# Performance work log

Measured on AMD Instinct MI355X. Metric: run time of the kernel, lower is better.

## Reference

```python
import jax, jax.numpy as jnp
import numpy as np

N = 50000   # nodes
E = 800000  # edges per metapath
P = 3       # num_meta_paths
H = 4       # heads
D = 64      # out_size per head
IN = H * D  # in_size = 256 (required by residual g_emb.flatten(1) + h)
EPS = 1e-5
NEG_SLOPE = 0.2  # DGL GATConv leaky_relu default


def setup_inputs() -> dict:
    key = jax.random.key(0)
    ks = jax.random.split(key, 7)
    h = jax.random.normal(ks[0], (N, IN), jnp.float32)
    path_mask = jnp.ones((N, P), jnp.float32)
    src = jax.random.randint(ks[1], (P, E), 0, N, jnp.int32)
    dst = jax.random.randint(ks[2], (P, E), 0, N, jnp.int32)
    # per-metapath GATConv params (bias=False)
    fc_w = jax.random.normal(ks[3], (P, IN, H * D), jnp.float32) * 0.05
    attn_l = jax.random.normal(ks[4], (P, H, D), jnp.float32) * 0.05
    attn_r = jax.random.normal(ks[5], (P, H, D), jnp.float32) * 0.05
    bn_gamma = jnp.ones((IN,), jnp.float32)
    bn_beta = jnp.zeros((IN,), jnp.float32)
    return {"h": h, "path_mask": path_mask, "src": src, "dst": dst,
            "fc_w": fc_w, "attn_l": attn_l, "attn_r": attn_r,
            "bn_gamma": bn_gamma, "bn_beta": bn_beta}


def _gat(h, src, dst, w, al, ar):
    # DGL GATConv: linear proj, additive attention, edge-softmax over dst neighborhoods
    feat = (h @ w).reshape(N, H, D)                       # [N,H,D]
    el = jnp.sum(feat * al, axis=-1)                      # [N,H]
    er = jnp.sum(feat * ar, axis=-1)                      # [N,H]
    e = jax.nn.leaky_relu(el[src] + er[dst], NEG_SLOPE)   # [E,H]
    # numerically-stable segment softmax over incoming edges of each dst node
    m = jax.ops.segment_max(e, dst, num_segments=N)       # [N,H]
    ex = jnp.exp(e - m[dst])
    denom = jax.ops.segment_sum(ex, dst, num_segments=N)  # [N,H]
    alpha = ex / denom[dst]                               # [E,H]
    out = jax.ops.segment_sum(alpha[:, :, None] * feat[src], dst, num_segments=N)  # [N,H,D]
    return jax.nn.relu(out), alpha


def _bn(x, gamma, beta):
    # BatchNorm1d in training mode: batch statistics over node dim
    mu = jnp.mean(x, axis=0)
    var = jnp.var(x, axis=0)
    return gamma * (x - mu) * jax.lax.rsqrt(var + EPS) + beta


def reference(h, path_mask, src, dst, fc_w, attn_l, attn_r, bn_gamma, bn_beta):
    embs, attns = [], []
    for p in range(P):
        o, a = _gat(h, src[p], dst[p], fc_w[p], attn_l[p], attn_r[p])
        embs.append(_bn(o.reshape(N, H * D) + h, bn_gamma, bn_beta))
        attns.append(jnp.mean(a, axis=1))  # mean over heads -> per-edge coef [E]
    sem = jnp.stack(embs, axis=1)                              # [N,P,IN]
    w = path_mask / jnp.sum(path_mask, axis=1, keepdims=True)  # masked mean weights [N,P]
    pooled = jnp.einsum('np,npd->nd', w, sem)                  # [N,IN]
    gat_attns = jnp.stack(attns)                               # [P,E] (sparse values; indices = src/dst)
    return pooled, w, gat_attns
```

## Files before the change

### kernel.cpp

```cpp
#include <hip/hip_runtime.h>
#include <stdint.h>

#define N_NODES 50000
#define N_EDGES 800000
#define N_PATHS 3
#define N_HEADS 4
#define IN_F 256
#define BN_EPS 1e-5f
#define NEG_SLOPE 0.2f
#define CAP 48
#define NB_PER_PATH 49
#define NB_TOT (N_PATHS * NB_PER_PATH)
#define REC_CAP 18432
#define BIN_EPB 4096
#define TOT_EDGES (N_PATHS * N_EDGES)
#define BIN_BLOCKS ((TOT_EDGES + BIN_EPB - 1) / BIN_EPB)

typedef short bf16x8 __attribute__((ext_vector_type(8)));
typedef float f32x4 __attribute__((ext_vector_type(4)));

__device__ inline unsigned short f2bf(float f) {
  unsigned u = __float_as_uint(f);
  unsigned r = (u + 0x7FFFu + ((u >> 16) & 1u)) >> 16;
  return (unsigned short)r;
}
__device__ inline float bf2f(unsigned short s) {
  return __uint_as_float(((unsigned)s) << 16);
}
__device__ inline float bfl(unsigned u) { return __uint_as_float(u << 16); }
__device__ inline float bfh(unsigned u) { return __uint_as_float(u & 0xFFFF0000u); }

__global__ __launch_bounds__(256) void k_zero(unsigned* p, int nwords) {
  int i = blockIdx.x * 256 + threadIdx.x;
  if (i < nwords) p[i] = 0u;
}

__global__ __launch_bounds__(256) void k_convert_w(const float* __restrict__ fcw,
                                                   unsigned short* __restrict__ wbf) {
  __shared__ float sh[32][33];
  int bt = blockIdx.x;
  int p = bt >> 6;
  int tile = bt & 63;
  int tk = tile >> 3, tn = tile & 7;
  const float* base = fcw + (size_t)p * IN_F * IN_F;
  unsigned short* ob = wbf + (size_t)p * IN_F * IN_F;
  int c = threadIdx.x & 31, r0 = threadIdx.x >> 5;
  #pragma unroll
  for (int it = 0; it < 4; ++it) {
    int r = r0 + it * 8;
    sh[r][c] = base[(size_t)(tk * 32 + r) * IN_F + tn * 32 + c];
  }
  __syncthreads();
  #pragma unroll
  for (int it = 0; it < 4; ++it) {
    int r = r0 + it * 8;
    ob[(size_t)(tn * 32 + r) * IN_F + tk * 32 + c] = f2bf(sh[c][r]);
  }
}

__global__ __launch_bounds__(256) void k_bin(const int* __restrict__ src, const int* __restrict__ dst,
                                             unsigned* __restrict__ gcurP, unsigned* __restrict__ grec) {
  __shared__ unsigned hist[NB_TOT];
  __shared__ unsigned lbase[NB_TOT];
  __shared__ unsigned gbase[NB_TOT];
  __shared__ unsigned lcur[NB_TOT];
  __shared__ unsigned scanbuf[256];
  __shared__ unsigned char sbuck[BIN_EPB];
  __shared__ unsigned stage[BIN_EPB];
  int t = threadIdx.x;
  int base = blockIdx.x * BIN_EPB;
  for (int i = t; i < NB_TOT; i += 256) { hist[i] = 0u; lcur[i] = 0u; }
  __syncthreads();

  unsigned rec[16];
  int bk[16];
  #pragma unroll
  for (int k = 0; k < 16; ++k) {
    int gid = base + t + k * 256;
    bk[k] = -1;
    if (gid < TOT_EDGES) {
      int s = src[gid], d = dst[gid];
      int p = (gid >= 2 * N_EDGES) ? 2 : ((gid >= N_EDGES) ? 1 : 0);
      int b = p * NB_PER_PATH + (d >> 10);
      bk[k] = b;
      rec[k] = (unsigned)s | ((unsigned)(d & 1023) << 17);
      atomicAdd(&hist[b], 1u);
    }
  }
  __syncthreads();
  for (int i = t; i < NB_TOT; i += 256)
    gbase[i] = hist[i] ? atomicAdd(&gcurP[i * 16], hist[i]) : 0u;
  scanbuf[t] = (t < NB_TOT) ? hist[t] : 0u;
  __syncthreads();
  for (int off = 1; off < 256; off <<= 1) {
    unsigned v = (t >= off) ? scanbuf[t - off] : 0u;
    __syncthreads();
    scanbuf[t] += v;
    __syncthreads();
  }
  if (t < NB_TOT) lbase[t] = scanbuf[t] - hist[t];
  __syncthreads();
  #pragma unroll
  for (int k = 0; k < 16; ++k) {
    if (bk[k] >= 0) {
      int b = bk[k];
      unsigned pos = atomicAdd(&lcur[b], 1u) + lbase[b];
      stage[pos] = rec[k];
      sbuck[pos] = (unsigned char)b;
    }
  }
  __syncthreads();
  int nblk = TOT_EDGES - base;
  if (nblk > BIN_EPB) nblk = BIN_EPB;
  for (int i = t; i < nblk; i += 256) {
    int b = sbuck[i];
    unsigned off = (unsigned)i - lbase[b];
    unsigned gpos = gbase[b] + off;
    if (gpos < REC_CAP) grec[(size_t)b * REC_CAP + gpos] = stage[i];
  }
}

__global__ __launch_bounds__(1024) void k_fine(const unsigned* __restrict__ gcurP,
                                               const unsigned* __restrict__ grec,
                                               unsigned short* __restrict__ slots,
                                               int* __restrict__ cnt) {
  __shared__ unsigned cur[1024];
  int b = blockIdx.x;
  int p = b / NB_PER_PATH;
  int nb0 = (b % NB_PER_PATH) << 10;
  int t = threadIdx.x;
  cur[t] = 0u;
  __syncthreads();
  unsigned M = gcurP[b * 16];
  if (M > REC_CAP) M = REC_CAP;
  const unsigned* rb = grec + (size_t)b * REC_CAP;
  for (unsigned i = t; i < M; i += 1024) {
    unsigned r = rb[i];
    int node = r >> 17;
    int srcv = r & 0x1FFFF;
    unsigned pos = atomicAdd(&cur[node], 1u);
    if (pos < CAP)
      slots[((size_t)(p * N_NODES + nb0 + node)) * CAP + pos] = (unsigned short)srcv;
  }
  __syncthreads();
  int node = nb0 + t;
  if (node < N_NODES) cnt[p * N_NODES + node] = (int)cur[t];
}

__global__ __launch_bounds__(256) void k_gemm(const float* __restrict__ h,
                                              const unsigned short* __restrict__ wbf,
                                              const float* __restrict__ attl,
                                              const float* __restrict__ attr,
                                              unsigned short* __restrict__ featbf,
                                              float* __restrict__ el,
                                              float* __restrict__ erd) {
  __shared__ unsigned short As[64 * 264];
  __shared__ unsigned short Bs[64 * 264];
  __shared__ float sal[256];
  __shared__ float sar[256];
  int m0 = blockIdx.x * 64;
  int p = blockIdx.y;
  int tid = threadIdx.x;
  const unsigned short* wptr = wbf + (size_t)p * IN_F * IN_F;

  sal[tid] = attl[p * 256 + tid];
  sar[tid] = attr[p * 256 + tid];
  for (int i = tid; i < 2048; i += 256) {
    int r = i >> 5, g = i & 31;
    int gr = m0 + r;
    uint4 o = make_uint4(0, 0, 0, 0);
    if (gr < N_NODES) {
      const float* hp = h + (size_t)gr * IN_F + g * 8;
      float4 v0 = *(const float4*)hp;
      float4 v1 = *(const float4*)(hp + 4);
      o.x = (unsigned)f2bf(v0.x) | ((unsigned)f2bf(v0.y) << 16);
      o.y = (unsigned)f2bf(v0.z) | ((unsigned)f2bf(v0.w) << 16);
      o.z = (unsigned)f2bf(v1.x) | ((unsigned)f2bf(v1.y) << 16);
      o.w = (unsigned)f2bf(v1.z) | ((unsigned)f2bf(v1.w) << 16);
    }
    *(uint4*)(&As[r * 264 + g * 8]) = o;
  }

  int wv = tid >> 6, lane = tid & 63;
  int l15 = lane & 15, quad = lane >> 4;
  const unsigned short* arow = &As[(wv * 16 + l15) * 264];
  size_t featbase = (size_t)p * N_NODES * IN_F;
  float* elp = el + (size_t)p * N_NODES * 4;
  float* erdp = erd + (size_t)p * N_NODES * 8;

  for (int c = 0; c < 4; ++c) {
    __syncthreads();
    for (int i = tid; i < 2048; i += 256) {
      int r = i >> 5, g = i & 31;
      *(uint4*)(&Bs[r * 264 + g * 8]) =
          *(const uint4*)(wptr + (size_t)(c * 64 + r) * IN_F + g * 8);
    }
    __syncthreads();

    f32x4 acc[4];
    #pragma unroll
    for (int i = 0; i < 4; ++i) acc[i] = (f32x4){0.f, 0.f, 0.f, 0.f};
    #pragma unroll
    for (int kb = 0; kb < 8; ++kb) {
      bf16x8 a = *(const bf16x8*)(arow + kb * 32 + quad * 8);
      #pragma unroll
      for (int nn = 0; nn < 4; ++nn) {
        bf16x8 b = *(const bf16x8*)(&Bs[(nn * 16 + l15) * 264 + kb * 32 + quad * 8]);
        acc[nn] = __builtin_amdgcn_mfma_f32_16x16x32_bf16(a, b, acc[nn], 0, 0, 0);
      }
    }
    #pragma unroll
    for (int nn = 0; nn < 4; ++nn)
      #pragma unroll
      for (int rg = 0; rg < 4; ++rg) {
        int grow = m0 + wv * 16 + quad * 4 + rg;
        if (grow < N_NODES)
          featbf[featbase + (size_t)grow * IN_F + c * 64 + nn * 16 + l15] = f2bf(acc[nn][rg]);
      }
    #pragma unroll
    for (int rg = 0; rg < 4; ++rg) {
      float a = 0.f, b = 0.f;
      #pragma unroll
      for (int nn = 0; nn < 4; ++nn) {
        float v = acc[nn][rg];
        int col = c * 64 + nn * 16 + l15;
        a += v * sal[col];
        b += v * sar[col];
      }
      a += __shfl_xor(a, 1); a += __shfl_xor(a, 2); a += __shfl_xor(a, 4); a += __shfl_xor(a, 8);
      b += __shfl_xor(b, 1); b += __shfl_xor(b, 2); b += __shfl_xor(b, 4); b += __shfl_xor(b, 8);
      int grow = m0 + wv * 16 + quad * 4 + rg;
      if (l15 == 0 && grow < N_NODES) {
        elp[(size_t)grow * 4 + c] = a;
        erdp[(size_t)grow * 8 + c] = b;
      }
    }
  }
}

__global__ __launch_bounds__(256) void k_gather(const int* __restrict__ cnt,
                                                const unsigned short* __restrict__ slots,
                                                const float* __restrict__ el,
                                                float* __restrict__ erd,
                                                const unsigned short* __restrict__ featbf,
                                                unsigned short* __restrict__ outbuf) {
  __shared__ float xs[4][4][CAP];
  __shared__ unsigned soff[4][CAP];
  int p = blockIdx.y;
  int tid = threadIdx.x;
  int wv = tid >> 6, lane = tid & 63;
  int node = blockIdx.x * 4 + wv;
  int b = p * N_NODES + node;
  int half = lane >> 5, lane32 = lane & 31;
  int head = lane32 >> 3;
  int m = cnt[b];
  if (m > CAP) m = CAP;
  const float* elp = el + (size_t)p * N_NODES * 4;
  float* erdp = erd + (size_t)p * N_NODES * 8;
  const unsigned short* sl = slots + (size_t)b * CAP;
  const char* fp_ = (const char*)featbf + (size_t)p * N_NODES * IN_F * 2 + lane32 * 16;

  {
    int headA = lane >> 4;
    float ern = erdp[(size_t)node * 8 + headA];
    for (int e = lane & 15; e < m; e += 16) {
      int s = (int)sl[e];
      if (headA == 0) soff[wv][e] = (unsigned)s * (unsigned)(IN_F * 2);
      float ev = elp[s * 4 + headA] + ern;
      ev = ev > 0.f ? ev : NEG_SLOPE * ev;
      xs[wv][headA][e] = __expf(ev);
    }
  }

  float a0 = 0.f, a1 = 0.f, a2 = 0.f, a3 = 0.f;
  float a4 = 0.f, a5 = 0.f, a6 = 0.f, a7 = 0.f, den = 0.f;
  int i = half;
  for (; i + 6 < m; i += 8) {
    unsigned o0 = soff[wv][i], o1 = soff[wv][i + 2], o2 = soff[wv][i + 4], o3 = soff[wv][i + 6];
    float x0 = xs[wv][head][i], x1 = xs[wv][head][i + 2];
    float x2 = xs[wv][head][i + 4], x3 = xs[wv][head][i + 6];
    uint4 f0 = *(const uint4*)(fp_ + o0);
    uint4 f1 = *(const uint4*)(fp_ + o1);
    uint4 f2 = *(const uint4*)(fp_ + o2);
    uint4 f3 = *(const uint4*)(fp_ + o3);
    den += (x0 + x1) + (x2 + x3);
    a0 += x0 * bfl(f0.x) + x1 * bfl(f1.x) + x2 * bfl(f2.x) + x3 * bfl(f3.x);
    a1 += x0 * bfh(f0.x) + x1 * bfh(f1.x) + x2 * bfh(f2.x) + x3 * bfh(f3.x);
    a2 += x0 * bfl(f0.y) + x1 * bfl(f1.y) + x2 * bfl(f2.y) + x3 * bfl(f3.y);
    a3 += x0 * bfh(f0.y) + x1 * bfh(f1.y) + x2 * bfh(f2.y) + x3 * bfh(f3.y);
    a4 += x0 * bfl(f0.z) + x1 * bfl(f1.z) + x2 * bfl(f2.z) + x3 * bfl(f3.z);
    a5 += x0 * bfh(f0.z) + x1 * bfh(f1.z) + x2 * bfh(f2.z) + x3 * bfh(f3.z);
    a6 += x0 * bfl(f0.w) + x1 * bfl(f1.w) + x2 * bfl(f2.w) + x3 * bfl(f3.w);
    a7 += x0 * bfh(f0.w) + x1 * bfh(f1.w) + x2 * bfh(f2.w) + x3 * bfh(f3.w);
  }
  for (; i + 2 < m; i += 4) {
    unsigned o0 = soff[wv][i], o1 = soff[wv][i + 2];
    float x0 = xs[wv][head][i], x1 = xs[wv][head][i + 2];
    uint4 f0 = *(const uint4*)(fp_ + o0);
    uint4 f1 = *(const uint4*)(fp_ + o1);
    den += x0 + x1;
    a0 += x0 * bfl(f0.x) + x1 * bfl(f1.x);
    a1 += x0 * bfh(f0.x) + x1 * bfh(f1.x);
    a2 += x0 * bfl(f0.y) + x1 * bfl(f1.y);
    a3 += x0 * bfh(f0.y) + x1 * bfh(f1.y);
    a4 += x0 * bfl(f0.z) + x1 * bfl(f1.z);
    a5 += x0 * bfh(f0.z) + x1 * bfh(f1.z);
    a6 += x0 * bfl(f0.w) + x1 * bfl(f1.w);
    a7 += x0 * bfh(f0.w) + x1 * bfh(f1.w);
  }
  for (; i < m; i += 2) {
    unsigned o0 = soff[wv][i];
    float x0 = xs[wv][head][i];
    uint4 f = *(const uint4*)(fp_ + o0);
    den += x0;
    a0 += x0 * bfl(f.x);
    a1 += x0 * bfh(f.x);
    a2 += x0 * bfl(f.y);
    a3 += x0 * bfh(f.y);
    a4 += x0 * bfl(f.z);
    a5 += x0 * bfh(f.z);
    a6 += x0 * bfl(f.w);
    a7 += x0 * bfh(f.w);
  }

  den += __shfl_xor(den, 32);
  a0 += __shfl_xor(a0, 32);
  a1 += __shfl_xor(a1, 32);
  a2 += __shfl_xor(a2, 32);
  a3 += __shfl_xor(a3, 32);
  a4 += __shfl_xor(a4, 32);
  a5 += __shfl_xor(a5, 32);
  a6 += __shfl_xor(a6, 32);
  a7 += __shfl_xor(a7, 32);
  if (half == 0) {
    float inv = den > 0.f ? 1.f / den : 0.f;
    float o0 = fmaxf(a0 * inv, 0.f), o1 = fmaxf(a1 * inv, 0.f);
    float o2 = fmaxf(a2 * inv, 0.f), o3 = fmaxf(a3 * inv, 0.f);
    float o4 = fmaxf(a4 * inv, 0.f), o5 = fmaxf(a5 * inv, 0.f);
    float o6 = fmaxf(a6 * inv, 0.f), o7 = fmaxf(a7 * inv, 0.f);
    uint4 u;
    u.x = (unsigned)f2bf(o0) | ((unsigned)f2bf(o1) << 16);
    u.y = (unsigned)f2bf(o2) | ((unsigned)f2bf(o3) << 16);
    u.z = (unsigned)f2bf(o4) | ((unsigned)f2bf(o5) << 16);
    u.w = (unsigned)f2bf(o6) | ((unsigned)f2bf(o7) << 16);
    *(uint4*)(outbuf + (size_t)b * IN_F + lane32 * 8) = u;
    if ((lane32 & 7) == 0) erdp[(size_t)node * 8 + 4 + head] = inv;
  }
}

__global__ __launch_bounds__(256) void k_attn(const int* __restrict__ src, const int* __restrict__ dst,
                                              const float* __restrict__ el,
                                              const float* __restrict__ erd,
                                              float* __restrict__ attn_out) {
  int eid = blockIdx.x * 256 + threadIdx.x;
  int p = eid / N_EDGES;
  int s = src[eid], t = dst[eid];
  const float* elp = el + (size_t)p * N_NODES * 4;
  const float* erdp = erd + (size_t)p * N_NODES * 8;
  float4 a = *(const float4*)(elp + (size_t)s * 4);
  float4 b = *(const float4*)(erdp + (size_t)t * 8);
  float4 idn = *(const float4*)(erdp + (size_t)t * 8 + 4);
  float4 e;
  e.x = a.x + b.x; e.x = e.x > 0.f ? e.x : NEG_SLOPE * e.x;
  e.y = a.y + b.y; e.y = e.y > 0.f ? e.y : NEG_SLOPE * e.y;
  e.z = a.z + b.z; e.z = e.z > 0.f ? e.z : NEG_SLOPE * e.z;
  e.w = a.w + b.w; e.w = e.w > 0.f ? e.w : NEG_SLOPE * e.w;
  attn_out[eid] = 0.25f * (__expf(e.x) * idn.x + __expf(e.y) * idn.y +
                           __expf(e.z) * idn.z + __expf(e.w) * idn.w);
}

__global__ __launch_bounds__(256) void k_bnstats3(const unsigned short* __restrict__ outbuf,
                                                  const float* __restrict__ h,
                                                  float* __restrict__ colsum, float* __restrict__ colsq) {
  int t = threadIdx.x;
  float s0 = 0.f, q0 = 0.f, s1 = 0.f, q1 = 0.f, s2 = 0.f, q2 = 0.f;
  for (int r = blockIdx.x; r < N_NODES; r += gridDim.x) {
    float hv = h[(size_t)r * IN_F + t];
    float v0 = bf2f(outbuf[(size_t)r * IN_F + t]) + hv;
    float v1 = bf2f(outbuf[((size_t)N_NODES + r) * IN_F + t]) + hv;
    float v2 = bf2f(outbuf[((size_t)2 * N_NODES + r) * IN_F + t]) + hv;
    s0 += v0; q0 += v0 * v0;
    s1 += v1; q1 += v1 * v1;
    s2 += v2; q2 += v2 * v2;
  }
  atomicAdd(&colsum[t], s0);
  atomicAdd(&colsq[t], q0);
  atomicAdd(&colsum[256 + t], s1);
  atomicAdd(&colsq[256 + t], q1);
  atomicAdd(&colsum[512 + t], s2);
  atomicAdd(&colsq[512 + t], q2);
}

__global__ __launch_bounds__(256) void k_bnapply3(const unsigned short* __restrict__ outbuf,
                                                  const float* __restrict__ h,
                                                  const float* __restrict__ colsum, const float* __restrict__ colsq,
                                                  const float* __restrict__ gamma, const float* __restrict__ beta,
                                                  const float* __restrict__ pmask,
                                                  float* __restrict__ pooled,
                                                  float* __restrict__ wout) {
  __shared__ float spm[3];
  int n = blockIdx.x, t = threadIdx.x;
  if (t < 3) spm[t] = pmask[n * 3 + t];
  __syncthreads();
  float ssum = spm[0] + spm[1] + spm[2];
  if (t < 3) wout[n * 3 + t] = spm[t] / ssum;
  const float invN = 1.f / (float)N_NODES;
  float hv = h[(size_t)n * IN_F + t];
  float g = gamma[t], bt = beta[t];
  float pv = 0.f;
  #pragma unroll
  for (int p = 0; p < 3; ++p) {
    float mu = colsum[p * 256 + t] * invN;
    float var = colsq[p * 256 + t] * invN - mu * mu;
    float rs = rsqrtf(var + BN_EPS);
    float v = bf2f(outbuf[((size_t)p * N_NODES + n) * IN_F + t]) + hv;
    float emb = g * (v - mu) * rs + bt;
    pv += (spm[p] / ssum) * emb;
  }
  pooled[(size_t)n * IN_F + t] = pv;
}

extern "C" void kernel_launch(void* const* d_in, const int* in_sizes, int n_in,
                              void* d_out, int out_size, void* d_ws, size_t ws_size,
                              hipStream_t stream) {
  const float* h     = (const float*)d_in[0];
  const float* pmask = (const float*)d_in[1];
  const int*   src   = (const int*)d_in[2];
  const int*   dst   = (const int*)d_in[3];
  const float* fcw   = (const float*)d_in[4];
  const float* attl  = (const float*)d_in[5];
  const float* attr  = (const float*)d_in[6];
  const float* gamma = (const float*)d_in[7];
  const float* beta  = (const float*)d_in[8];

  float* out_pooled = (float*)d_out;
  float* out_w = out_pooled + (size_t)N_NODES * IN_F;
  float* out_attn = out_w + (size_t)N_NODES * N_PATHS;

  char* wp = (char*)d_ws;
  auto carve = [&](size_t bytes) {
    char* r = wp;
    wp += (bytes + 255) & ~(size_t)255;
    return r;
  };
  unsigned short* featbf = (unsigned short*)carve((size_t)N_PATHS * N_NODES * IN_F * 2);
  unsigned short* wbf    = (unsigned short*)carve((size_t)N_PATHS * IN_F * IN_F * 2);
  unsigned short* outbuf = (unsigned short*)carve((size_t)N_PATHS * N_NODES * IN_F * 2);
  char* grec_base = carve((size_t)NB_TOT * REC_CAP * 4);
  unsigned* grec = (unsigned*)grec_base;
  float* el  = (float*)grec_base;
  float* erd = el + (size_t)N_PATHS * N_NODES * 4;
  unsigned short* slots = (unsigned short*)carve((size_t)N_PATHS * N_NODES * CAP * 2);
  int* cnt = (int*)carve((size_t)N_PATHS * N_NODES * 4);
  char* zbase = wp;
  unsigned* gcurP = (unsigned*)carve((size_t)NB_TOT * 16 * 4);
  float* colsum = (float*)carve((size_t)N_PATHS * IN_F * 4);
  float* colsq  = (float*)carve((size_t)N_PATHS * IN_F * 4);
  int zero_words = (int)((wp - zbase) / 4);

  k_convert_w<<<N_PATHS * 64, 256, 0, stream>>>(fcw, wbf);
  k_zero<<<(zero_words + 255) / 256, 256, 0, stream>>>((unsigned*)zbase, zero_words);
  k_bin<<<BIN_BLOCKS, 256, 0, stream>>>(src, dst, gcurP, grec);
  k_fine<<<NB_TOT, 1024, 0, stream>>>(gcurP, grec, slots, cnt);
  k_gemm<<<dim3((N_NODES + 63) / 64, N_PATHS), 256, 0, stream>>>(h, wbf, attl, attr,
                                                                 featbf, el, erd);
  k_gather<<<dim3(N_NODES / 4, N_PATHS), 256, 0, stream>>>(cnt, slots, el, erd, featbf, outbuf);
  k_attn<<<TOT_EDGES / 256, 256, 0, stream>>>(src, dst, el, erd, out_attn);
  k_bnstats3<<<512, 256, 0, stream>>>(outbuf, h, colsum, colsq);
  k_bnapply3<<<N_NODES, 256, 0, stream>>>(outbuf, h, colsum, colsq, gamma, beta, pmask,
                                          out_pooled, out_w);
}
```

Measured before the change: 539.9 us.

## Split fine binning into quarter-node blocks and grid-stride the BN apply kernel

k_fine now launches four blocks per coarse bin. Each block rescans all records of the bin but only handles nodes in its 256-node quarter, which raises parallelism from 147 blocks to 588. The trade-off is that every record is read four times. k_bnapply3 becomes a grid-stride loop over nodes with 1024 blocks, so the per-column BN mean and rsqrt are computed once per thread instead of once per node, and the shared-memory sync for the path mask is removed.

Measured after the change: 543.1 us. About the same (+0.6%).

```diff
diff --git a/kernel.cpp b/kernel.cpp
--- a/kernel.cpp
+++ b/kernel.cpp
@@ -124,12 +124,13 @@
                                                const unsigned* __restrict__ grec,
                                                unsigned short* __restrict__ slots,
                                                int* __restrict__ cnt) {
-  __shared__ unsigned cur[1024];
-  int b = blockIdx.x;
+  __shared__ unsigned cur[256];
+  int blk = blockIdx.x;
+  int b = blk >> 2, hf = blk & 3;
   int p = b / NB_PER_PATH;
   int nb0 = (b % NB_PER_PATH) << 10;
   int t = threadIdx.x;
-  cur[t] = 0u;
+  if (t < 256) cur[t] = 0u;
   __syncthreads();
   unsigned M = gcurP[b * 16];
   if (M > REC_CAP) M = REC_CAP;
@@ -137,14 +138,18 @@
   for (unsigned i = t; i < M; i += 1024) {
     unsigned r = rb[i];
     int node = r >> 17;
-    int srcv = r & 0x1FFFF;
-    unsigned pos = atomicAdd(&cur[node], 1u);
-    if (pos < CAP)
-      slots[((size_t)(p * N_NODES + nb0 + node)) * CAP + pos] = (unsigned short)srcv;
-  }
-  __syncthreads();
-  int node = nb0 + t;
-  if (node < N_NODES) cnt[p * N_NODES + node] = (int)cur[t];
+    if ((node >> 8) == hf) {
+      int srcv = r & 0x1FFFF;
+      unsigned pos = atomicAdd(&cur[node & 255], 1u);
+      if (pos < CAP)
+        slots[((size_t)(p * N_NODES + nb0 + node)) * CAP + pos] = (unsigned short)srcv;
+    }
+  }
+  __syncthreads();
+  if (t < 256) {
+    int node = nb0 + (hf << 8) + t;
+    if (node < N_NODES) cnt[p * N_NODES + node] = (int)cur[t];
+  }
 }
 
 __global__ __launch_bounds__(256) void k_gemm(const float* __restrict__ h,
@@ -398,26 +403,31 @@
                                                   const float* __restrict__ pmask,
                                                   float* __restrict__ pooled,
                                                   float* __restrict__ wout) {
-  __shared__ float spm[3];
-  int n = blockIdx.x, t = threadIdx.x;
-  if (t < 3) spm[t] = pmask[n * 3 + t];
-  __syncthreads();
-  float ssum = spm[0] + spm[1] + spm[2];
-  if (t < 3) wout[n * 3 + t] = spm[t] / ssum;
+  int t = threadIdx.x;
   const float invN = 1.f / (float)N_NODES;
-  float hv = h[(size_t)n * IN_F + t];
   float g = gamma[t], bt = beta[t];
-  float pv = 0.f;
-  #pragma unroll
-  for (int p = 0; p < 3; ++p) {
-    float mu = colsum[p * 256 + t] * invN;
-    float var = colsq[p * 256 + t] * invN - mu * mu;
-    float rs = rsqrtf(var + BN_EPS);
-    float v = bf2f(outbuf[((size_t)p * N_NODES + n) * IN_F + t]) + hv;
-    float emb = g * (v - mu) * rs + bt;
-    pv += (spm[p] / ssum) * emb;
-  }
-  pooled[(size_t)n * IN_F + t] = pv;
+  float mu0 = colsum[t] * invN;
+  float rs0 = rsqrtf(colsq[t] * invN - mu0 * mu0 + BN_EPS);
+  float mu1 = colsum[256 + t] * invN;
+  float rs1 = rsqrtf(colsq[256 + t] * invN - mu1 * mu1 + BN_EPS);
+  float mu2 = colsum[512 + t] * invN;
+  float rs2 = rsqrtf(colsq[512 + t] * invN - mu2 * mu2 + BN_EPS);
+  for (int n = blockIdx.x; n < N_NODES; n += gridDim.x) {
+    float p0 = pmask[n * 3], p1 = pmask[n * 3 + 1], p2 = pmask[n * 3 + 2];
+    float inv_s = 1.f / (p0 + p1 + p2);
+    float w0 = p0 * inv_s, w1 = p1 * inv_s, w2 = p2 * inv_s;
+    if (t == 0) {
+      wout[n * 3] = w0; wout[n * 3 + 1] = w1; wout[n * 3 + 2] = w2;
+    }
+    float hv = h[(size_t)n * IN_F + t];
+    float v0 = bf2f(outbuf[(size_t)n * IN_F + t]) + hv;
+    float v1 = bf2f(outbuf[((size_t)N_NODES + n) * IN_F + t]) + hv;
+    float v2 = bf2f(outbuf[((size_t)2 * N_NODES + n) * IN_F + t]) + hv;
+    float pv = w0 * (g * (v0 - mu0) * rs0 + bt) +
+               w1 * (g * (v1 - mu1) * rs1 + bt) +
+               w2 * (g * (v2 - mu2) * rs2 + bt);
+    pooled[(size_t)n * IN_F + t] = pv;
+  }
 }
 
 extern "C" void kernel_launch(void* const* d_in, const int* in_sizes, int n_in,
@@ -461,12 +471,12 @@
   k_convert_w<<<N_PATHS * 64, 256, 0, stream>>>(fcw, wbf);
   k_zero<<<(zero_words + 255) / 256, 256, 0, stream>>>((unsigned*)zbase, zero_words);
   k_bin<<<BIN_BLOCKS, 256, 0, stream>>>(src, dst, gcurP, grec);
-  k_fine<<<NB_TOT, 1024, 0, stream>>>(gcurP, grec, slots, cnt);
+  k_fine<<<NB_TOT * 4, 1024, 0, stream>>>(gcurP, grec, slots, cnt);
   k_gemm<<<dim3((N_NODES + 63) / 64, N_PATHS), 256, 0, stream>>>(h, wbf, attl, attr,
                                                                  featbf, el, erd);
   k_gather<<<dim3(N_NODES / 4, N_PATHS), 256, 0, stream>>>(cnt, slots, el, erd, featbf, outbuf);
   k_attn<<<TOT_EDGES / 256, 256, 0, stream>>>(src, dst, el, erd, out_attn);
   k_bnstats3<<<512, 256, 0, stream>>>(outbuf, h, colsum, colsq);
-  k_bnapply3<<<N_NODES, 256, 0, stream>>>(outbuf, h, colsum, colsq, gamma, beta, pmask,
-                                          out_pooled, out_w);
-}
+  k_bnapply3<<<1024, 256, 0, stream>>>(outbuf, h, colsum, colsq, gamma, beta, pmask,
+                                       out_pooled, out_w);
+}
```
